# Performance work log

Measured on AMD Instinct MI355X. Metric: run time of the kernel, lower is better.

The kernel has to match this reference:

```python
import jax, jax.numpy as jnp
import numpy as np

B, T, D = 2, 2048, 1024
N, H = 16, 64  # num_heads, head_dim


def setup_inputs() -> dict:
    key = jax.random.key(0)
    ks = jax.random.split(key, 8)
    glorot = lambda k, shape, fan_in, fan_out: jax.random.uniform(
        k, shape, jnp.float32, -1.0, 1.0) * np.sqrt(6.0 / (fan_in + fan_out))
    return {
        "q": jax.random.normal(ks[0], (B, T, D), jnp.float32),
        "v": jax.random.normal(ks[1], (B, T, D), jnp.float32),
        "k": jax.random.normal(ks[2], (B, T, D), jnp.float32),
        "w_query": glorot(ks[3], (D, N, H), D, N * H),
        "b_query": jnp.zeros((N, 1, H), jnp.float32),
        "w_value": glorot(ks[4], (D, N, H), D, N * H),
        "b_value": jnp.zeros((N, 1, H), jnp.float32),
        "w_key": glorot(ks[5], (D, N, H), D, N * H),
        "b_key": jnp.zeros((N, 1, H), jnp.float32),
        "w_projection": glorot(ks[6], (N, D, H), N * H, D),
        "b_projection": jnp.zeros((1, D), jnp.float32),
    }


def reference(q, v, k, w_query, b_query, w_value, b_value, w_key, b_key,
              w_projection, b_projection):
    # QKV projections: [B,T,D] x [D,N,H] -> [B,N,T,H]
    query = jnp.einsum('btd,dnh->bnth', q, w_query) + b_query
    value = jnp.einsum('btd,dnh->bnth', v, w_value) + b_value
    key_p = jnp.einsum('btd,dnh->bnth', k, w_key) + b_key
    # Scaled dot-product attention, scores divided by sqrt(head_dim)
    scale = 1.0 / jnp.sqrt(jnp.asarray(H, query.dtype))
    scores = jnp.einsum('bnth,bnsh->bnts', query, key_p) * scale  # [B,N,T,T]
    weights = jax.nn.softmax(scores, axis=-1)
    attn = jnp.einsum('bnts,bnsh->bnth', weights, value)
    # Output projection: [B,N,T,H] x [N,D,H] -> [B,T,D]
    out = jnp.einsum('bnth,ndh->btd', attn, w_projection) + b_projection
    return out
```

## Files before the change

### kernel.cpp

```cpp
#include <hip/hip_runtime.h>
#include <hip/hip_bf16.h>
#include <cstdint>
#include <cstddef>


typedef __attribute__((ext_vector_type(8))) short short8;
typedef __attribute__((ext_vector_type(4))) float floatx4;
typedef __attribute__((ext_vector_type(8))) unsigned short ushort8;

#define EXP2F(x) __builtin_amdgcn_exp2f(x)

static __device__ __forceinline__ unsigned short f2bf(float f) {
    union { float f; unsigned int u; } v; v.f = f;
    unsigned int r = v.u + 0x7fffu + ((v.u >> 16) & 1u);
    return (unsigned short)(r >> 16);
}
static __device__ __forceinline__ unsigned int pk2bf(float lo, float hi) {
    __hip_bfloat162 t = __float22bfloat162_rn(make_float2(lo, hi));
    union { __hip_bfloat162 h; unsigned int u; } c; c.h = t;
    return c.u;
}
static __device__ __forceinline__ void gl_lds16(const unsigned short* g, unsigned short* l) {
    __builtin_amdgcn_global_load_lds(
        (const __attribute__((address_space(1))) unsigned int*)g,
        (__attribute__((address_space(3))) unsigned int*)l, 16, 0, 0);
}
static __device__ __forceinline__ void gl_lds16f(const float* g, float* l) {
    __builtin_amdgcn_global_load_lds(
        (const __attribute__((address_space(1))) unsigned int*)g,
        (__attribute__((address_space(3))) unsigned int*)l, 16, 0, 0);
}

__global__ __launch_bounds__(256) void mha_prep_w(
    const float* __restrict__ wq, const float* __restrict__ wk, const float* __restrict__ wv,
    const float* __restrict__ wp,
    unsigned short* __restrict__ wqT, unsigned short* __restrict__ wkT,
    unsigned short* __restrict__ wvT, unsigned short* __restrict__ wp2)
{
    __shared__ float tile[32][33];
    int z = blockIdx.z;
    int tid = threadIdx.x;
    if (z < 3) {
        const float* src = z == 0 ? wq : (z == 1 ? wk : wv);
        unsigned short* dst = z == 0 ? wqT : (z == 1 ? wkT : wvT);
        int n0 = blockIdx.x * 32, d0 = blockIdx.y * 32;
        int tx = tid & 31, ty = tid >> 5;
        #pragma unroll
        for (int j = 0; j < 4; ++j)
            tile[ty + j * 8][tx] = src[(size_t)(d0 + ty + j * 8) * 1024 + n0 + tx];
        __syncthreads();
        #pragma unroll
        for (int j = 0; j < 4; ++j)
            dst[(size_t)(n0 + ty + j * 8) * 1024 + d0 + tx] = f2bf(tile[tx][ty + j * 8]);
    } else {
        int bid = blockIdx.x + blockIdx.y * 32;
        int base = bid * 1024 + tid;
        #pragma unroll
        for (int i = 0; i < 4; ++i) {
            int idx = base + i * 256;
            int n = idx >> 16, d = (idx >> 6) & 1023, h = idx & 63;
            wp2[(size_t)d * 1024 + n * 64 + h] = f2bf(wp[idx]);
        }
    }
}

__global__ __launch_bounds__(256) void gemm_qkv128(
    const float* __restrict__ A0, const float* __restrict__ A1, const float* __restrict__ A2,
    const unsigned short* __restrict__ W0, const unsigned short* __restrict__ W1,
    const unsigned short* __restrict__ W2,
    const float* __restrict__ b0, const float* __restrict__ b1, const float* __restrict__ b2,
    unsigned short* __restrict__ O0, unsigned short* __restrict__ O1, unsigned short* __restrict__ O2,
    float qscale)
{
    __shared__ float Asf[128 * 32];
    __shared__ unsigned short Bs[128 * 32];
    int bm = blockIdx.x, by = blockIdx.y;
    int mat = by >> 3, nt = by & 7;
    const float* A           = mat == 0 ? A0 : (mat == 1 ? A1 : A2);
    const unsigned short* WT = mat == 0 ? W0 : (mat == 1 ? W1 : W2);
    const float* bias        = mat == 0 ? b0 : (mat == 1 ? b1 : b2);
    unsigned short* Out      = mat == 0 ? O0 : (mat == 1 ? O1 : O2);
    float scale = (mat == 0) ? qscale : 1.0f;
    int vmode = (mat == 2);

    int tid = threadIdx.x;
    int w = tid >> 6, lane = tid & 63, c15 = lane & 15, quad = lane >> 4;
    int wm = w >> 1, wn = w & 1;

    const float* gA[4]; float* lA[4];
    #pragma unroll
    for (int i = 0; i < 4; ++i) {
        int s = (w * 4 + i) * 64 + lane;
        int row = s >> 3, cl4 = (s & 7) ^ ((row & 3) << 1);
        gA[i] = A + (size_t)(bm * 128 + row) * 1024 + cl4 * 4;
        lA[i] = &Asf[s * 4];
    }
    const unsigned short* gB[2]; unsigned short* lB[2];
    #pragma unroll
    for (int i = 0; i < 2; ++i) {
        int s = (w * 2 + i) * 64 + lane;
        gB[i] = WT + (size_t)(nt * 128 + (s >> 2)) * 1024 + (s & 3) * 8;
        lB[i] = &Bs[s * 8];
    }

    floatx4 acc[4][4];
    #pragma unroll
    for (int mi = 0; mi < 4; ++mi)
        #pragma unroll
        for (int ni = 0; ni < 4; ++ni) acc[mi][ni] = (floatx4){0.f, 0.f, 0.f, 0.f};

    for (int kt = 0; kt < 32; ++kt) {
        __syncthreads();
        #pragma unroll
        for (int i = 0; i < 4; ++i) gl_lds16f(gA[i] + kt * 32, lA[i]);
        #pragma unroll
        for (int i = 0; i < 2; ++i) gl_lds16(gB[i] + kt * 32, lB[i]);
        __syncthreads();
        short8 af[4], bfr[4];
        #pragma unroll
        for (int mi = 0; mi < 4; ++mi) {
            int row = wm * 64 + mi * 16 + c15;
            int oc = (quad ^ (row & 3)) * 8;
            float4 a0 = *(const float4*)&Asf[row * 32 + oc];
            float4 a1 = *(const float4*)&Asf[row * 32 + oc + 4];
            union { uint4 u; short8 s; } cv;
            cv.u.x = pk2bf(a0.x, a0.y); cv.u.y = pk2bf(a0.z, a0.w);
            cv.u.z = pk2bf(a1.x, a1.y); cv.u.w = pk2bf(a1.z, a1.w);
            af[mi] = cv.s;
        }
        #pragma unroll
        for (int ni = 0; ni < 4; ++ni)
            bfr[ni] = *(const short8*)&Bs[(wn * 64 + ni * 16 + c15) * 32 + quad * 8];
        #pragma unroll
        for (int mi = 0; mi < 4; ++mi)
            #pragma unroll
            for (int ni = 0; ni < 4; ++ni)
                acc[mi][ni] = __builtin_amdgcn_mfma_f32_16x16x32_bf16(af[mi], bfr[ni], acc[mi][ni], 0, 0, 0);
    }
    #pragma unroll
    for (int mi = 0; mi < 4; ++mi)
        #pragma unroll
        for (int ni = 0; ni < 4; ++ni)
            #pragma unroll
            for (int r = 0; r < 4; ++r) {
                int row = bm * 128 + wm * 64 + mi * 16 + quad * 4 + r;
                int col = nt * 128 + wn * 64 + ni * 16 + c15;
                float val = (acc[mi][ni][r] + bias[col]) * scale;
                int b = row >> 11, t = row & 2047, n = col >> 6, h = col & 63;
                if (vmode)
                    Out[((size_t)(b * 16 + n) * 64 + h) * 2048 + t] = f2bf(val);
                else
                    Out[((size_t)(b * 16 + n) * 2048 + t) * 64 + h] = f2bf(val);
            }
}

__global__ __launch_bounds__(256) void mha_flash3(
    const unsigned short* __restrict__ Qp, const unsigned short* __restrict__ Kp,
    const unsigned short* __restrict__ Vt, unsigned short* __restrict__ attnb)
{
    __shared__ unsigned short Ks[64 * 72];
    __shared__ unsigned short Vs[64 * 72];
    __shared__ unsigned short Pl[4][32 * 72];

    int bi = blockIdx.x;
    int xcd = bi & 7, j = bi >> 3;
    int bn = xcd * 4 + (j >> 4), qt = j & 15;
    int b = bn >> 4, n = bn & 15;
    int tid = threadIdx.x;
    int w = tid >> 6, lane = tid & 63, c15 = lane & 15, quad = lane >> 4;

    const unsigned short* Qb = Qp + (size_t)bn * 2048 * 64;
    const unsigned short* Kb = Kp + (size_t)bn * 2048 * 64;
    const unsigned short* Vb = Vt + (size_t)bn * 64 * 2048;

    int qbase = qt * 128 + w * 32;

    short8 bQ[2][2];
    #pragma unroll
    for (int tni = 0; tni < 2; ++tni)
        #pragma unroll
        for (int kc = 0; kc < 2; ++kc)
            bQ[tni][kc] = *(const short8*)(Qb + (size_t)(qbase + tni * 16 + c15) * 64 + kc * 32 + quad * 8);

    float l_i[2] = {0.f, 0.f};
    floatx4 o[2][4];
    #pragma unroll
    for (int i = 0; i < 2; ++i)
        #pragma unroll
        for (int j2 = 0; j2 < 4; ++j2) o[i][j2] = (floatx4){0.f, 0.f, 0.f, 0.f};

    unsigned short* Pw = &Pl[w][0];
    int srow = tid >> 3, scc = tid & 7;

    ushort8 kreg[2], vreg[2];
    #pragma unroll
    for (int i = 0; i < 2; ++i) {
        kreg[i] = *(const ushort8*)(Kb + (size_t)(srow + i * 32) * 64 + scc * 8);
        vreg[i] = *(const ushort8*)(Vb + (size_t)(srow + i * 32) * 2048 + scc * 8);
    }

    for (int it = 0; it < 32; ++it) {
        __syncthreads();
        #pragma unroll
        for (int i = 0; i < 2; ++i) {
            *(ushort8*)&Ks[(srow + i * 32) * 72 + scc * 8] = kreg[i];
            *(ushort8*)&Vs[(srow + i * 32) * 72 + scc * 8] = vreg[i];
        }
        __syncthreads();
        if (it < 31) {
            int s1 = (it + 1) * 64;
            #pragma unroll
            for (int i = 0; i < 2; ++i) {
                kreg[i] = *(const ushort8*)(Kb + (size_t)(s1 + srow + i * 32) * 64 + scc * 8);
                vreg[i] = *(const ushort8*)(Vb + (size_t)(srow + i * 32) * 2048 + s1 + scc * 8);
            }
        }

        floatx4 sc[4][2];
        #pragma unroll
        for (int smi = 0; smi < 4; ++smi) {
            short8 a0 = *(const short8*)&Ks[(smi * 16 + c15) * 72 + quad * 8];
            short8 a1 = *(const short8*)&Ks[(smi * 16 + c15) * 72 + 32 + quad * 8];
            #pragma unroll
            for (int tni = 0; tni < 2; ++tni) {
                floatx4 t = (floatx4){0.f, 0.f, 0.f, 0.f};
                t = __builtin_amdgcn_mfma_f32_16x16x32_bf16(a0, bQ[tni][0], t, 0, 0, 0);
                t = __builtin_amdgcn_mfma_f32_16x16x32_bf16(a1, bQ[tni][1], t, 0, 0, 0);
                sc[smi][tni] = t;
            }
        }
        #pragma unroll
        for (int tni = 0; tni < 2; ++tni) {
            float rs = 0.f;
            #pragma unroll
            for (int smi = 0; smi < 4; ++smi) {
                float p0 = EXP2F(sc[smi][tni][0]);
                float p1 = EXP2F(sc[smi][tni][1]);
                float p2 = EXP2F(sc[smi][tni][2]);
                float p3 = EXP2F(sc[smi][tni][3]);
                rs += (p0 + p1) + (p2 + p3);
                uint2 pw;
                pw.x = pk2bf(p0, p1);
                pw.y = pk2bf(p2, p3);
                *(uint2*)&Pw[(tni * 16 + c15) * 72 + smi * 16 + quad * 4] = pw;
            }
            l_i[tni] += rs;
        }
        short8 bv[4][2];
        #pragma unroll
        for (int hni = 0; hni < 4; ++hni)
            #pragma unroll
            for (int kc = 0; kc < 2; ++kc)
                bv[hni][kc] = *(const short8*)&Vs[(hni * 16 + c15) * 72 + kc * 32 + quad * 8];
        #pragma unroll
        for (int tmi = 0; tmi < 2; ++tmi) {
            short8 ap0 = *(const short8*)&Pw[(tmi * 16 + c15) * 72 + quad * 8];
            short8 ap1 = *(const short8*)&Pw[(tmi * 16 + c15) * 72 + 32 + quad * 8];
            #pragma unroll
            for (int hni = 0; hni < 4; ++hni) {
                o[tmi][hni] = __builtin_amdgcn_mfma_f32_16x16x32_bf16(ap0, bv[hni][0], o[tmi][hni], 0, 0, 0);
                o[tmi][hni] = __builtin_amdgcn_mfma_f32_16x16x32_bf16(ap1, bv[hni][1], o[tmi][hni], 0, 0, 0);
            }
        }
    }
    float lf[2];
    #pragma unroll
    for (int tmi = 0; tmi < 2; ++tmi) {
        float s = l_i[tmi];
        s += __shfl_xor(s, 16, 64);
        s += __shfl_xor(s, 32, 64);
        lf[tmi] = s;
    }
    #pragma unroll
    for (int tmi = 0; tmi < 2; ++tmi)
        #pragma unroll
        for (int r = 0; r < 4; ++r) {
            float linv = 1.0f / __shfl(lf[tmi], quad * 4 + r, 64);
            int t = qbase + tmi * 16 + quad * 4 + r;
            #pragma unroll
            for (int hni = 0; hni < 4; ++hni) {
                int col = n * 64 + hni * 16 + c15;
                attnb[(size_t)(b * 2048 + t) * 1024 + col] = f2bf(o[tmi][hni][r] * linv);
            }
        }
}

__global__ __launch_bounds__(256) void gemm_out64v2(
    const unsigned short* __restrict__ A, const unsigned short* __restrict__ BT,
    const float* __restrict__ bias, float* __restrict__ out)
{
    __shared__ unsigned short As[64 * 64];
    __shared__ unsigned short Bs[128 * 64];
    int g = blockIdx.x + (blockIdx.y << 6);
    int nt = g & 7, bm = g >> 3;
    int tid = threadIdx.x;
    int w = tid >> 6, lane = tid & 63, c15 = lane & 15, quad = lane >> 4;
    int wm = w >> 1, wn = w & 1;

    const unsigned short* gA[2]; unsigned short* lA[2];
    const unsigned short* gB[4]; unsigned short* lB[4];
    #pragma unroll
    for (int i = 0; i < 2; ++i) {
        int s = (w * 2 + i) * 64 + lane;
        int row = s >> 3, cl = (s & 7) ^ (row & 7);
        gA[i] = A + (size_t)(bm * 64 + row) * 1024 + cl * 8;
        lA[i] = &As[s * 8];
    }
    #pragma unroll
    for (int i = 0; i < 4; ++i) {
        int s = (w * 4 + i) * 64 + lane;
        int row = s >> 3, cl = (s & 7) ^ (row & 7);
        gB[i] = BT + (size_t)(nt * 128 + row) * 1024 + cl * 8;
        lB[i] = &Bs[s * 8];
    }

    floatx4 acc[2][4];
    #pragma unroll
    for (int mi = 0; mi < 2; ++mi)
        #pragma unroll
        for (int ni = 0; ni < 4; ++ni) acc[mi][ni] = (floatx4){0.f, 0.f, 0.f, 0.f};

    for (int kt = 0; kt < 16; ++kt) {
        __syncthreads();
        #pragma unroll
        for (int i = 0; i < 2; ++i) gl_lds16(gA[i] + kt * 64, lA[i]);
        #pragma unroll
        for (int i = 0; i < 4; ++i) gl_lds16(gB[i] + kt * 64, lB[i]);
        __syncthreads();
        #pragma unroll
        for (int kc = 0; kc < 2; ++kc) {
            short8 af[2], bfr[4];
            #pragma unroll
            for (int mi = 0; mi < 2; ++mi) {
                int row = wm * 32 + mi * 16 + c15;
                af[mi] = *(const short8*)&As[row * 64 + (((kc * 4 + quad) ^ (row & 7)) * 8)];
            }
            #pragma unroll
            for (int ni = 0; ni < 4; ++ni) {
                int row = wn * 64 + ni * 16 + c15;
                bfr[ni] = *(const short8*)&Bs[row * 64 + (((kc * 4 + quad) ^ (row & 7)) * 8)];
            }
            #pragma unroll
            for (int mi = 0; mi < 2; ++mi)
                #pragma unroll
                for (int ni = 0; ni < 4; ++ni)
                    acc[mi][ni] = __builtin_amdgcn_mfma_f32_16x16x32_bf16(af[mi], bfr[ni], acc[mi][ni], 0, 0, 0);
        }
    }
    #pragma unroll
    for (int mi = 0; mi < 2; ++mi)
        #pragma unroll
        for (int ni = 0; ni < 4; ++ni)
            #pragma unroll
            for (int r = 0; r < 4; ++r) {
                int row = bm * 64 + wm * 32 + mi * 16 + quad * 4 + r;
                int col = nt * 128 + wn * 64 + ni * 16 + c15;
                out[(size_t)row * 1024 + col] = acc[mi][ni][r] + bias[col];
            }
}

extern "C" void kernel_launch(void* const* d_in, const int* in_sizes, int n_in,
                              void* d_out, int out_size, void* d_ws, size_t ws_size,
                              hipStream_t stream)
{
    const float* q  = (const float*)d_in[0];
    const float* v  = (const float*)d_in[1];
    const float* k  = (const float*)d_in[2];
    const float* wq = (const float*)d_in[3];
    const float* bq = (const float*)d_in[4];
    const float* wv = (const float*)d_in[5];
    const float* bv = (const float*)d_in[6];
    const float* wk = (const float*)d_in[7];
    const float* bk = (const float*)d_in[8];
    const float* wp = (const float*)d_in[9];
    const float* bp = (const float*)d_in[10];
    float* out = (float*)d_out;

    char* ws = (char*)d_ws;
    unsigned short* wqT  = (unsigned short*)(ws + (size_t)0);
    unsigned short* wkT  = (unsigned short*)(ws + ((size_t)2  << 20));
    unsigned short* wvT  = (unsigned short*)(ws + ((size_t)4  << 20));
    unsigned short* wp2  = (unsigned short*)(ws + ((size_t)6  << 20));
    unsigned short* Qp   = (unsigned short*)(ws + ((size_t)8  << 20));
    unsigned short* Kp   = (unsigned short*)(ws + ((size_t)16 << 20));
    unsigned short* Vtp  = (unsigned short*)(ws + ((size_t)24 << 20));
    unsigned short* attnb= (unsigned short*)(ws + ((size_t)32 << 20));

    const float qscale = 0.125f * 1.44269504088896f;

    hipLaunchKernelGGL(mha_prep_w, dim3(32, 32, 4), dim3(256), 0, stream,
                       wq, wk, wv, wp, wqT, wkT, wvT, wp2);
    hipLaunchKernelGGL(gemm_qkv128, dim3(32, 24), dim3(256), 0, stream,
                       q, k, v, wqT, wkT, wvT, bq, bk, bv, Qp, Kp, Vtp, qscale);
    hipLaunchKernelGGL(mha_flash3, dim3(512), dim3(256), 0, stream, Qp, Kp, Vtp, attnb);
    hipLaunchKernelGGL(gemm_out64v2, dim3(64, 8), dim3(256), 0, stream, attnb, wp2, bp, out);
}
```

Before: 233.5 us.

## Register-prefetch QKV GEMM A/B tiles and convert A to bf16 before LDS store

The QKV projection GEMM no longer uses direct global-to-LDS loads. Each thread now prefetches the next k-tile of fp32 A and bf16 W into registers while MFMAs run on the current tile. A is converted to bf16 once per element before the LDS write, instead of being converted redundantly by every wave that reads it. This halves LDS footprint and read traffic for A and overlaps global loads with compute, at the cost of extra registers and dropping the swizzled layout, which may cause LDS bank conflicts.

New measurement: 235.4 us. No clear change (+0.8%).

```diff
diff --git a/kernel.cpp b/kernel.cpp
--- a/kernel.cpp
+++ b/kernel.cpp
@@ -21,11 +21,6 @@
     return c.u;
 }
 static __device__ __forceinline__ void gl_lds16(const unsigned short* g, unsigned short* l) {
-    __builtin_amdgcn_global_load_lds(
-        (const __attribute__((address_space(1))) unsigned int*)g,
-        (__attribute__((address_space(3))) unsigned int*)l, 16, 0, 0);
-}
-static __device__ __forceinline__ void gl_lds16f(const float* g, float* l) {
     __builtin_amdgcn_global_load_lds(
         (const __attribute__((address_space(1))) unsigned int*)g,
         (__attribute__((address_space(3))) unsigned int*)l, 16, 0, 0);
@@ -72,7 +67,7 @@
     unsigned short* __restrict__ O0, unsigned short* __restrict__ O1, unsigned short* __restrict__ O2,
     float qscale)
 {
-    __shared__ float Asf[128 * 32];
+    __shared__ unsigned short As[128 * 32];
     __shared__ unsigned short Bs[128 * 32];
     int bm = blockIdx.x, by = blockIdx.y;
     int mat = by >> 3, nt = by & 7;
@@ -87,18 +82,13 @@
     int w = tid >> 6, lane = tid & 63, c15 = lane & 15, quad = lane >> 4;
     int wm = w >> 1, wn = w & 1;
 
-    const float* gA[4]; float* lA[4];
-    #pragma unroll
-    for (int i = 0; i < 4; ++i) {
-        int s = (w * 4 + i) * 64 + lane;
-        int row = s >> 3, cl4 = (s & 7) ^ ((row & 3) << 1);
-        gA[i] = A + (size_t)(bm * 128 + row) * 1024 + cl4 * 4;
-        lA[i] = &Asf[s * 4];
-    }
+    const float* gAf[2]; unsigned short* lA[2];
     const unsigned short* gB[2]; unsigned short* lB[2];
     #pragma unroll
     for (int i = 0; i < 2; ++i) {
         int s = (w * 2 + i) * 64 + lane;
+        gAf[i] = A + (size_t)(bm * 128 + (s >> 2)) * 1024 + (s & 3) * 8;
+        lA[i] = &As[s * 8];
         gB[i] = WT + (size_t)(nt * 128 + (s >> 2)) * 1024 + (s & 3) * 8;
         lB[i] = &Bs[s * 8];
     }
@@ -109,25 +99,40 @@
         #pragma unroll
         for (int ni = 0; ni < 4; ++ni) acc[mi][ni] = (floatx4){0.f, 0.f, 0.f, 0.f};
 
+    float4 af4[2][2];
+    ushort8 bq[2];
+    #pragma unroll
+    for (int i = 0; i < 2; ++i) {
+        af4[i][0] = *(const float4*)(gAf[i]);
+        af4[i][1] = *(const float4*)(gAf[i] + 4);
+        bq[i]     = *(const ushort8*)(gB[i]);
+    }
+
     for (int kt = 0; kt < 32; ++kt) {
         __syncthreads();
         #pragma unroll
-        for (int i = 0; i < 4; ++i) gl_lds16f(gA[i] + kt * 32, lA[i]);
-        #pragma unroll
-        for (int i = 0; i < 2; ++i) gl_lds16(gB[i] + kt * 32, lB[i]);
-        __syncthreads();
+        for (int i = 0; i < 2; ++i) {
+            uint4 pk;
+            pk.x = pk2bf(af4[i][0].x, af4[i][0].y);
+            pk.y = pk2bf(af4[i][0].z, af4[i][0].w);
+            pk.z = pk2bf(af4[i][1].x, af4[i][1].y);
+            pk.w = pk2bf(af4[i][1].z, af4[i][1].w);
+            *(uint4*)lA[i] = pk;
+            *(ushort8*)lB[i] = bq[i];
+        }
+        __syncthreads();
+        if (kt < 31) {
+            #pragma unroll
+            for (int i = 0; i < 2; ++i) {
+                af4[i][0] = *(const float4*)(gAf[i] + (kt + 1) * 32);
+                af4[i][1] = *(const float4*)(gAf[i] + (kt + 1) * 32 + 4);
+                bq[i]     = *(const ushort8*)(gB[i] + (kt + 1) * 32);
+            }
+        }
         short8 af[4], bfr[4];
         #pragma unroll
-        for (int mi = 0; mi < 4; ++mi) {
-            int row = wm * 64 + mi * 16 + c15;
-            int oc = (quad ^ (row & 3)) * 8;
-            float4 a0 = *(const float4*)&Asf[row * 32 + oc];
-            float4 a1 = *(const float4*)&Asf[row * 32 + oc + 4];
-            union { uint4 u; short8 s; } cv;
-            cv.u.x = pk2bf(a0.x, a0.y); cv.u.y = pk2bf(a0.z, a0.w);
-            cv.u.z = pk2bf(a1.x, a1.y); cv.u.w = pk2bf(a1.z, a1.w);
-            af[mi] = cv.s;
-        }
+        for (int mi = 0; mi < 4; ++mi)
+            af[mi] = *(const short8*)&As[(wm * 64 + mi * 16 + c15) * 32 + quad * 8];
         #pragma unroll
         for (int ni = 0; ni < 4; ++ni)
             bfr[ni] = *(const short8*)&Bs[(wn * 64 + ni * 16 + c15) * 32 + quad * 8];
```
